# Kernel optimization log

Measured on AMD Instinct MI355X. Metric: run time of the kernel, lower is better.

The kernel has to match this reference:

```python
import jax, jax.numpy as jnp
import numpy as np

D = 512      # d_model
H = 8        # n_head
NL = 3       # encoder layers
FF = 2048    # torch TransformerEncoderLayer default dim_feedforward
HID = 256    # hidden_size
ACT = 12     # action_size
NOBJ = 89    # num_objects
BAND = 17    # tril(diagonal=-17) -> keys older than 16 steps banned


def setup_inputs() -> dict:
    key = jax.random.key(0)
    ks = iter(jax.random.split(key, 48))
    rn = lambda shape, s=0.02: jax.random.normal(next(ks), shape, jnp.float32) * s
    b, seq = 16, 512
    inp = {
        'state_input': jax.random.normal(next(ks), (b, seq, 3, 16, 16), jnp.float32),
        'goal_input': jax.random.normal(next(ks), (b, seq, 300), jnp.float32),
        # encoders (stand-ins for obs_enc / lang_enc)
        'W_obs': rn((256, 3 * 16 * 16)), 'b_obs': rn((256,)),
        'W_lang': rn((256, 300)), 'b_lang': rn((256,)),
        # input projection 512 -> 512
        'W_in': rn((D, 512)), 'b_in': rn((D,)),
        # per-layer transformer params, stacked on layer dim
        'Wqkv': rn((NL, 3 * D, D)), 'bqkv': rn((NL, 3 * D)),
        'Wo': rn((NL, D, D)), 'bo': rn((NL, D)),
        'W1': rn((NL, FF, D)), 'b1': rn((NL, FF)),
        'W2': rn((NL, D, FF)), 'b2': rn((NL, D)),
        'g1': jnp.ones((NL, D)), 'bt1': jnp.zeros((NL, D)),
        'g2': jnp.ones((NL, D)), 'bt2': jnp.zeros((NL, D)),
        # output heads
        'W_outp': rn((HID, D)), 'b_outp': rn((HID,)),
        'W_a1': rn((ACT, HID)), 'b_a1': rn((ACT,)),
        'W_a2': rn((NOBJ, HID)), 'b_a2': rn((NOBJ,)),
    }
    return inp


def _ln(y, g, bt):
    m = y.mean(-1, keepdims=True)
    v = y.var(-1, keepdims=True)
    return (y - m) / jnp.sqrt(v + 1e-5) * g + bt


def _encoder(x, mask_add, Wqkv, bqkv, Wo, bo, W1, b1, W2, b2, g1, bt1, g2, bt2):
    b, n, _ = x.shape
    dh = D // H
    scale = 1.0 / np.sqrt(dh)
    for l in range(NL):
        qkv = x @ Wqkv[l].T + bqkv[l]
        q, k, v = jnp.split(qkv, 3, axis=-1)
        hd = lambda t: t.reshape(b, n, H, dh).transpose(0, 2, 1, 3)  # [b,h,n,dh]
        q, k, v = hd(q), hd(k), hd(v)
        sc = jnp.einsum('bhqd,bhkd->bhqk', q, k) * scale + mask_add
        a = jax.nn.softmax(sc, axis=-1)
        o = jnp.einsum('bhqk,bhkd->bhqd', a, v).transpose(0, 2, 1, 3).reshape(b, n, D)
        o = o @ Wo[l].T + bo[l]
        x = _ln(x + o, g1[l], bt1[l])             # post-LN (torch default)
        f = jax.nn.relu(x @ W1[l].T + b1[l]) @ W2[l].T + b2[l]
        x = _ln(x + f, g2[l], bt2[l])
    return x


def reference(state_input, goal_input, W_obs, b_obs, W_lang, b_lang, W_in, b_in,
              Wqkv, bqkv, Wo, bo, W1, b1, W2, b2, g1, bt1, g2, bt2,
              W_outp, b_outp, W_a1, b_a1, W_a2, b_a2):
    b, s = state_input.shape[:2]
    st = state_input.reshape(b, s, -1) @ W_obs.T + b_obs          # obs_enc
    lg = goal_input @ W_lang.T + b_lang                            # lang_enc
    x = jnp.concatenate([st, lg], axis=-1) @ W_in.T + b_in        # [b,s,D]
    # key padding mask; sentinel token appended (causal_mask=False branch)
    pad = ~jnp.any(goal_input != -1, axis=-1)                      # [b,s]
    pad = jnp.concatenate([pad, jnp.zeros((b, 1), bool)], axis=1)
    x = jnp.concatenate([x, jnp.zeros((b, 1, D), x.dtype)], axis=1)
    n = s + 1
    i = jnp.arange(n)
    # banned: tril(-17) | triu(1)  -> attend only to keys in [i-16, i]
    mask2 = ((i[:, None] - i[None, :]) >= BAND) | (i[None, :] > i[:, None])
    banned = mask2[None, None, :, :] | pad[:, None, None, :]
    mask_add = jnp.where(banned, jnp.float32(-1e9), jnp.float32(0.0))
    x = _encoder(x, mask_add, Wqkv, bqkv, Wo, bo, W1, b1, W2, b2, g1, bt1, g2, bt2)
    out = x[:, :-1, :]                                             # drop sentinel
    h = out @ W_outp.T + b_outp
    l1 = h @ W_a1.T + b_a1
    l2 = h @ W_a2.T + b_a2
    return jnp.concatenate([l1, l2], axis=-1)                      # [b,s,101]
```

## Files before the change

kernel.cpp:

```cpp
#include <hip/hip_runtime.h>

#define D 512
#define H 8
#define NL 3
#define FFD 2048
#define HID 256
#define BAND 17
#define BATCH 16
#define SEQ 512
#define MTOK (BATCH * SEQ)
#define NOUT 101
#define NOUTP 128

typedef unsigned short u16;
typedef __attribute__((ext_vector_type(8))) short short8;
typedef __attribute__((ext_vector_type(4))) float f32x4;
typedef __attribute__((ext_vector_type(8))) unsigned short u16x8;

__device__ inline float bf2f(u16 u) {
    union { unsigned int i; float f; } x; x.i = ((unsigned int)u) << 16; return x.f;
}
__device__ inline u16 f2bf(float f) {
    union { float f; unsigned int i; } x; x.f = f;
    unsigned int r = x.i + 0x7fffu + ((x.i >> 16) & 1u);
    return (u16)(r >> 16);
}

__device__ __forceinline__ void gload_lds16(const u16* g, u16* l) {
    __builtin_amdgcn_global_load_lds(
        (const __attribute__((address_space(1))) unsigned int*)(g),
        (__attribute__((address_space(3))) unsigned int*)(l),
        16, 0, 0);
}

#define BM 128
#define BN 128
#define BK 32

__global__ __launch_bounds__(512) void gemm_kernel(
    const u16* __restrict__ A, int lda,
    const u16* __restrict__ B, int ldb,
    const float* __restrict__ bias,
    float* __restrict__ Cf0, float* __restrict__ Cf1, int ldcf,
    u16* __restrict__ Cb, int ldcb,
    int M, int N, int K, int relu)
{
    __shared__ u16 As[3][BM * BK];
    __shared__ u16 Bs[3][BN * BK];
    const int tid  = threadIdx.x;
    const int lane = tid & 63;
    const int wv   = tid >> 6;
    const int wr = wv >> 2, wc = wv & 3;

    const int nb  = gridDim.x * gridDim.y;
    const int bid = blockIdx.y * gridDim.x + blockIdx.x;
    const int tile = (bid & 7) * (nb >> 3) + (bid >> 3);
    const int m0 = (tile / gridDim.x) * BM;
    const int n0 = (tile % gridDim.x) * BN;
    const int kz = blockIdx.z * K;

    f32x4 acc[4][2] = {};

    const int srow = lane >> 2;
    const int schunk = (lane & 3) ^ (srow & 3);
    const size_t aoff = (size_t)(m0 + wv * 16 + srow) * lda + kz + schunk * 8;
    const size_t boff = (size_t)(n0 + wv * 16 + srow) * ldb + kz + schunk * 8;

    const int frow = lane & 15;
    const int q    = lane >> 4;
    const int rcol = ((q ^ (frow & 3)) << 3);

    #define STAGE(buf, k0)                                             \
        do {                                                           \
            gload_lds16(A + aoff + (k0), &As[buf][wv * 16 * BK]);      \
            gload_lds16(B + boff + (k0), &Bs[buf][wv * 16 * BK]);      \
        } while (0)

    #define COMPUTE(buf)                                                            \
        do {                                                                        \
            short8 af[4], bf[2];                                                    \
            _Pragma("unroll")                                                       \
            for (int i = 0; i < 4; ++i)                                             \
                af[i] = *(const short8*)&As[buf][(wr * 64 + i * 16 + frow) * BK + rcol]; \
            _Pragma("unroll")                                                       \
            for (int j = 0; j < 2; ++j)                                             \
                bf[j] = *(const short8*)&Bs[buf][(wc * 32 + j * 16 + frow) * BK + rcol]; \
            _Pragma("unroll")                                                       \
            for (int i = 0; i < 4; ++i)                                             \
                _Pragma("unroll")                                                   \
                for (int j = 0; j < 2; ++j)                                         \
                    acc[i][j] = __builtin_amdgcn_mfma_f32_16x16x32_bf16(            \
                        af[i], bf[j], acc[i][j], 0, 0, 0);                          \
        } while (0)

    const int nt = K >> 5;
    STAGE(0, 0);
    STAGE(1, 32);
    int cur = 0;
    for (int t = 0; t < nt - 2; ++t) {
        int s = cur + 2; if (s >= 3) s -= 3;
        STAGE(s, (t + 2) << 5);
        asm volatile("s_waitcnt vmcnt(4)" ::: "memory");
        __builtin_amdgcn_s_barrier();
        __builtin_amdgcn_sched_barrier(0);
        COMPUTE(cur);
        __builtin_amdgcn_s_barrier();
        ++cur; if (cur >= 3) cur = 0;
    }
    asm volatile("s_waitcnt vmcnt(2)" ::: "memory");
    __builtin_amdgcn_s_barrier();
    __builtin_amdgcn_sched_barrier(0);
    COMPUTE(cur);
    __builtin_amdgcn_s_barrier();
    ++cur; if (cur >= 3) cur = 0;
    asm volatile("s_waitcnt vmcnt(0)" ::: "memory");
    __builtin_amdgcn_s_barrier();
    __builtin_amdgcn_sched_barrier(0);
    COMPUTE(cur);

    #undef STAGE
    #undef COMPUTE

    float* Cf = blockIdx.z ? Cf1 : Cf0;
    const bool addb = (bias != nullptr) && (blockIdx.z == 0);

    const int crow0 = (lane >> 4) * 4;
    const int ccol  = lane & 15;
    #pragma unroll
    for (int j = 0; j < 2; ++j) {
        int gcol = n0 + wc * 32 + j * 16 + ccol;
        if (gcol >= N) continue;
        float bv = addb ? bias[gcol] : 0.f;
        #pragma unroll
        for (int i = 0; i < 4; ++i) {
            #pragma unroll
            for (int r = 0; r < 4; ++r) {
                int grow = m0 + wr * 64 + i * 16 + crow0 + r;
                float v = acc[i][j][r] + bv;
                if (relu) v = fmaxf(v, 0.f);
                if (Cf) Cf[(size_t)grow * ldcf + gcol] = v;
                if (Cb) Cb[(size_t)grow * ldcb + gcol] = f2bf(v);
            }
        }
    }
}

#define CHUNK 128
#define KSLOT 144
#define VT_LD 152

__global__ __launch_bounds__(512) void attn_kernel(
    const u16* __restrict__ qkv, const unsigned char* __restrict__ pad,
    u16* __restrict__ o)
{
    __shared__ u16 Vt[64 * VT_LD];
    __shared__ u16 Pl[8 * 16 * 40];
    __shared__ unsigned char padl[KSLOT];

    const int tid = threadIdx.x, lane = tid & 63, wv = tid >> 6;
    const int b = blockIdx.z, h = blockIdx.y, c0 = blockIdx.x * CHUNK;
    const u16* base = qkv + (size_t)b * SEQ * (3 * D);

    for (int s = tid; s < KSLOT * 4; s += 512) {
        int t = s >> 2, dq = (s & 3) * 16;
        int j = c0 - 16 + t; if (j < 0) j = 0;
        const u16* vrow = base + (size_t)j * (3 * D) + 2 * D + h * 64 + dq;
        u16 tmp[16];
        *(u16x8*)&tmp[0] = *(const u16x8*)&vrow[0];
        *(u16x8*)&tmp[8] = *(const u16x8*)&vrow[8];
        #pragma unroll
        for (int d = 0; d < 16; ++d)
            Vt[(dq + d) * VT_LD + t] = tmp[d];
    }
    if (tid < KSLOT) {
        int j = c0 - 16 + tid;
        padl[tid] = (j >= 0) ? pad[b * SEQ + j] : (unsigned char)1;
    }
    __syncthreads();

    const int qi0 = wv * 16;
    const int i0  = c0 + qi0;
    const int frow = lane & 15;
    const int g    = lane >> 4;
    const int kg8  = g * 8;
    const int g4   = g * 4;

    short8 qf[2];
    #pragma unroll
    for (int kk = 0; kk < 2; ++kk)
        qf[kk] = *(const short8*)&base[(size_t)(i0 + frow) * (3 * D) + h * 64 + kk * 32 + kg8];

    f32x4 sacc[2] = {};
    #pragma unroll
    for (int jb = 0; jb < 2; ++jb) {
        int jrow = i0 - 16 + jb * 16 + frow; if (jrow < 0) jrow = 0;
        const u16* kbase = base + (size_t)jrow * (3 * D) + D + h * 64;
        #pragma unroll
        for (int kk = 0; kk < 2; ++kk) {
            short8 kf = *(const short8*)&kbase[kk * 32 + kg8];
            sacc[jb] = __builtin_amdgcn_mfma_f32_16x16x32_bf16(qf[kk], kf, sacc[jb], 0, 0, 0);
        }
    }

    float sv[2][4];
    #pragma unroll
    for (int jb = 0; jb < 2; ++jb) {
        int s = jb * 16 + frow;
        int jg = i0 - 16 + s;
        bool padk = (jg < 0) || padl[qi0 + s];
        #pragma unroll
        for (int r = 0; r < 4; ++r) {
            int qq = g4 + r;
            bool banned = (s < qq) || (s > qq + 16) || padk;
            sv[jb][r] = sacc[jb][r] * 0.125f + (banned ? -1e9f : 0.f);
        }
    }

    float ex[2][4], rdn[4];
    #pragma unroll
    for (int r = 0; r < 4; ++r) {
        float m = fmaxf(sv[0][r], sv[1][r]);
        #pragma unroll
        for (int off = 1; off < 16; off <<= 1) m = fmaxf(m, __shfl_xor(m, off));
        float e0 = __expf(sv[0][r] - m);
        float e1 = __expf(sv[1][r] - m);
        float dsum = e0 + e1;
        #pragma unroll
        for (int off = 1; off < 16; off <<= 1) dsum += __shfl_xor(dsum, off);
        ex[0][r] = e0; ex[1][r] = e1;
        rdn[r] = 1.f / dsum;
    }

    u16* Pw = &Pl[wv * 640];
    #pragma unroll
    for (int jb = 0; jb < 2; ++jb)
        #pragma unroll
        for (int r = 0; r < 4; ++r)
            Pw[(g4 + r) * 40 + jb * 16 + frow] = f2bf(ex[jb][r]);
    short8 pa = *(const short8*)&Pw[frow * 40 + kg8];

    f32x4 oacc[4] = {};
    #pragma unroll
    for (int nb = 0; nb < 4; ++nb) {
        short8 vf = *(const short8*)&Vt[(nb * 16 + frow) * VT_LD + qi0 + kg8];
        oacc[nb] = __builtin_amdgcn_mfma_f32_16x16x32_bf16(pa, vf, oacc[nb], 0, 0, 0);
    }

    #pragma unroll
    for (int r = 0; r < 4; ++r) {
        size_t row = (size_t)(b * SEQ + i0 + g4 + r);
        #pragma unroll
        for (int nb = 0; nb < 4; ++nb)
            o[row * D + h * 64 + nb * 16 + frow] = f2bf(oacc[nb][r] * rdn[r]);
    }
}

__global__ __launch_bounds__(256) void resln_kernel(
    const u16* __restrict__ xin,
    const float* __restrict__ d0, const float* __restrict__ d1,
    const float* __restrict__ g, const float* __restrict__ bt,
    u16* __restrict__ xb)
{
    int row  = blockIdx.x * 4 + (threadIdx.x >> 6);
    int lane = threadIdx.x & 63;
    const f32x4* r0 = (const f32x4*)(d0 + (size_t)row * D);
    const f32x4* r1 = (const f32x4*)(d1 + (size_t)row * D);
    u16x8 xv = *(const u16x8*)(xin + (size_t)row * D + lane * 8);

    f32x4 y0 = r0[lane * 2]     + r1[lane * 2];
    f32x4 y1 = r0[lane * 2 + 1] + r1[lane * 2 + 1];
    #pragma unroll
    for (int c = 0; c < 4; ++c) { y0[c] += bf2f(xv[c]); y1[c] += bf2f(xv[c + 4]); }

    float s = 0.f, s2 = 0.f;
    #pragma unroll
    for (int c = 0; c < 4; ++c) {
        s  += y0[c] + y1[c];
        s2 += y0[c] * y0[c] + y1[c] * y1[c];
    }
    #pragma unroll
    for (int off = 32; off > 0; off >>= 1) {
        s  += __shfl_xor(s, off);
        s2 += __shfl_xor(s2, off);
    }
    float mean = s * (1.f / D);
    float var  = s2 * (1.f / D) - mean * mean;
    float inv  = rsqrtf(fmaxf(var, 0.f) + 1e-5f);

    f32x4 gv0 = ((const f32x4*)g)[lane * 2],  gv1 = ((const f32x4*)g)[lane * 2 + 1];
    f32x4 bv0 = ((const f32x4*)bt)[lane * 2], bv1 = ((const f32x4*)bt)[lane * 2 + 1];
    u16x8 ob;
    #pragma unroll
    for (int c = 0; c < 4; ++c) {
        ob[c]     = f2bf((y0[c] - mean) * inv * gv0[c] + bv0[c]);
        ob[c + 4] = f2bf((y1[c] - mean) * inv * gv1[c] + bv1[c]);
    }
    *(u16x8*)(xb + (size_t)row * D + lane * 8) = ob;
}

__global__ __launch_bounds__(256) void pad_kernel(
    const float* __restrict__ goal, unsigned char* __restrict__ pad)
{
    int row  = blockIdx.x * 4 + (threadIdx.x >> 6);
    int lane = threadIdx.x & 63;
    const f32x4* gr = (const f32x4*)(goal + (size_t)row * 300);
    bool any = false;
    for (int c4 = lane; c4 < 75; c4 += 64) {
        f32x4 v = gr[c4];
        any |= (v[0] != -1.f) | (v[1] != -1.f) | (v[2] != -1.f) | (v[3] != -1.f);
    }
    unsigned long long b = __ballot(any);
    if (lane == 0) pad[row] = (b == 0ull) ? 1 : 0;
}

struct CvtJob { const float* src; u16* dstb; float* dstf; int n; int mode; };
struct CvtArgs { CvtJob j[15]; int blk0[16]; };

__global__ __launch_bounds__(256) void cvt_kernel(CvtArgs a) {
    const int bx = blockIdx.x;
    int jid = 0;
    #pragma unroll 1
    while (jid < 14 && bx >= a.blk0[jid + 1]) ++jid;
    const CvtJob jb = a.j[jid];
    const int i0 = (bx - a.blk0[jid]) * 2048 + threadIdx.x * 8;
    if (i0 >= jb.n) return;

    if (jb.mode == 0) {
        if (i0 + 8 <= jb.n) {
            f32x4 v0 = *(const f32x4*)(jb.src + i0);
            f32x4 v1 = *(const f32x4*)(jb.src + i0 + 4);
            u16x8 o;
            #pragma unroll
            for (int c = 0; c < 4; ++c) { o[c] = f2bf(v0[c]); o[c + 4] = f2bf(v1[c]); }
            *(u16x8*)(jb.dstb + i0) = o;
        } else {
            for (int e = 0; e < 8 && i0 + e < jb.n; ++e) jb.dstb[i0 + e] = f2bf(jb.src[i0 + e]);
        }
    } else if (jb.mode == 2) {
        int r = (int)((unsigned)i0 / 320u);
        int c = i0 - r * 320;
        const float* s = jb.src + (size_t)r * 300 + c;
        u16x8 o;
        if (c + 8 <= 300) {
            f32x4 v0 = *(const f32x4*)s;
            f32x4 v1 = *(const f32x4*)(s + 4);
            #pragma unroll
            for (int cc = 0; cc < 4; ++cc) { o[cc] = f2bf(v0[cc]); o[cc + 4] = f2bf(v1[cc]); }
        } else {
            #pragma unroll
            for (int e = 0; e < 8; ++e) o[e] = (c + e < 300) ? f2bf(s[e]) : (u16)0;
        }
        *(u16x8*)(jb.dstb + i0) = o;
    } else if (jb.mode == 1) {
        for (int e = 0; e < 8 && i0 + e < jb.n; ++e) jb.dstf[i0 + e] = jb.src[i0 + e];
    } else {
        u16x8 z = {0, 0, 0, 0, 0, 0, 0, 0};
        *(u16x8*)(jb.dstb + i0) = z;
    }
}


extern "C" void kernel_launch(void* const* d_in, const int* in_sizes, int n_in,
                              void* d_out, int out_size, void* d_ws, size_t ws_size,
                              hipStream_t stream)
{
    const float* state  = (const float*)d_in[0];
    const float* goal   = (const float*)d_in[1];
    const float* W_obs  = (const float*)d_in[2];
    const float* b_obs  = (const float*)d_in[3];
    const float* W_lang = (const float*)d_in[4];
    const float* b_lang = (const float*)d_in[5];
    const float* W_in   = (const float*)d_in[6];
    const float* b_in   = (const float*)d_in[7];
    const float* Wqkv   = (const float*)d_in[8];
    const float* bqkv   = (const float*)d_in[9];
    const float* Wo     = (const float*)d_in[10];
    const float* bo     = (const float*)d_in[11];
    const float* W1     = (const float*)d_in[12];
    const float* b1     = (const float*)d_in[13];
    const float* W2     = (const float*)d_in[14];
    const float* b2     = (const float*)d_in[15];
    const float* g1     = (const float*)d_in[16];
    const float* bt1    = (const float*)d_in[17];
    const float* g2     = (const float*)d_in[18];
    const float* bt2    = (const float*)d_in[19];
    const float* W_outp = (const float*)d_in[20];
    const float* b_outp = (const float*)d_in[21];
    const float* W_a1   = (const float*)d_in[22];
    const float* b_a1   = (const float*)d_in[23];
    const float* W_a2   = (const float*)d_in[24];
    const float* b_a2   = (const float*)d_in[25];

    char* ws = (char*)d_ws;
    size_t off = 0;
    auto alloc = [&](size_t bytes) -> void* {
        void* p = ws + off;
        off = (off + bytes + 255) & ~(size_t)255;
        return p;
    };

    u16* wqkv_b  = (u16*)alloc((size_t)NL * 1536 * D * 2);
    u16* wo_b    = (u16*)alloc((size_t)NL * D * D * 2);
    u16* w1_b    = (u16*)alloc((size_t)NL * FFD * D * 2);
    u16* w2_b    = (u16*)alloc((size_t)NL * D * FFD * 2);
    u16* wobs_b  = (u16*)alloc((size_t)256 * 768 * 2);
    u16* wlang_b = (u16*)alloc((size_t)256 * 320 * 2);
    u16* win_b   = (u16*)alloc((size_t)D * D * 2);
    u16* woutp_b = (u16*)alloc((size_t)HID * D * 2);
    u16* wa_b    = (u16*)alloc((size_t)NOUTP * HID * 2);
    float* ba_f  = (float*)alloc((size_t)NOUT * 4);
    u16* state_b = (u16*)alloc((size_t)MTOK * 768 * 2);
    u16* goal_b  = (u16*)alloc((size_t)MTOK * 320 * 2);
    u16* feat_b  = (u16*)alloc((size_t)MTOK * D * 2);
    u16* x_b     = (u16*)alloc((size_t)MTOK * D * 2);
    u16* qkv_b   = (u16*)alloc((size_t)MTOK * 3 * D * 2);
    u16* o_b     = (u16*)alloc((size_t)MTOK * D * 2);
    float* delta_f = (float*)alloc((size_t)MTOK * D * 4);
    u16* h1_b    = (u16*)alloc((size_t)MTOK * FFD * 2);
    u16* hout_b  = (u16*)alloc((size_t)MTOK * HID * 2);
    unsigned char* pad_u8 = (unsigned char*)alloc(MTOK);
    float* delta2_f = (float*)state_b;
    (void)ws_size; (void)in_sizes; (void)n_in; (void)out_size;

    CvtArgs ca;
    int nj = 0, blks = 0;
    auto addj = [&](const float* s, u16* db, float* df, int n, int mode) {
        ca.j[nj].src = s; ca.j[nj].dstb = db; ca.j[nj].dstf = df;
        ca.j[nj].n = n; ca.j[nj].mode = mode;
        ca.blk0[nj] = blks;
        blks += (n + 2047) / 2048;
        ++nj;
    };
    addj(state,  state_b, nullptr, MTOK * 768, 0);
    addj(goal,   goal_b,  nullptr, MTOK * 320, 2);
    addj(Wqkv,   wqkv_b,  nullptr, NL * 1536 * D, 0);
    addj(Wo,     wo_b,    nullptr, NL * D * D, 0);
    addj(W1,     w1_b,    nullptr, NL * FFD * D, 0);
    addj(W2,     w2_b,    nullptr, NL * D * FFD, 0);
    addj(W_obs,  wobs_b,  nullptr, 256 * 768, 0);
    addj(W_lang, wlang_b, nullptr, 256 * 320, 2);
    addj(W_in,   win_b,   nullptr, D * D, 0);
    addj(W_outp, woutp_b, nullptr, HID * D, 0);
    addj(W_a1,   wa_b,            nullptr, 12 * HID, 0);
    addj(W_a2,   wa_b + 12 * HID, nullptr, 89 * HID, 0);
    addj(nullptr, wa_b + NOUT * HID, nullptr, (NOUTP - NOUT) * HID, 3);
    addj(b_a1,   nullptr, ba_f,      12, 1);
    addj(b_a2,   nullptr, ba_f + 12, 89, 1);
    ca.blk0[nj] = blks;
    cvt_kernel<<<blks, 256, 0, stream>>>(ca);

    pad_kernel<<<MTOK / 4, 256, 0, stream>>>(goal, pad_u8);

    auto gemm = [&](const u16* A, int lda, const u16* B, int ldb, const float* bias,
                    float* Cf0, float* Cf1, int ldcf, u16* Cb, int ldcb,
                    int N, int K, int relu, int ksplit) {
        dim3 grid((N + BN - 1) / BN, MTOK / BM, ksplit);
        gemm_kernel<<<grid, 512, 0, stream>>>(A, lda, B, ldb, bias, Cf0, Cf1, ldcf,
                                              Cb, ldcb, MTOK, N, K / ksplit, relu);
    };

    gemm(state_b, 768, wobs_b, 768, b_obs, nullptr, nullptr, 0, feat_b, D, 256, 768, 0, 1);
    gemm(goal_b, 320, wlang_b, 320, b_lang, nullptr, nullptr, 0, feat_b + 256, D, 256, 320, 0, 1);
    gemm(feat_b, D, win_b, D, b_in, nullptr, nullptr, 0, x_b, D, D, D, 0, 1);

    for (int l = 0; l < NL; ++l) {
        gemm(x_b, D, wqkv_b + (size_t)l * 1536 * D, D, bqkv + l * 1536,
             nullptr, nullptr, 0, qkv_b, 3 * D, 3 * D, D, 0, 1);
        {
            dim3 grid(SEQ / CHUNK, H, BATCH);
            attn_kernel<<<grid, 512, 0, stream>>>(qkv_b, pad_u8, o_b);
        }
        gemm(o_b, D, wo_b + (size_t)l * D * D, D, bo + l * D,
             delta_f, delta2_f, D, nullptr, 0, D, D, 0, 2);
        resln_kernel<<<MTOK / 4, 256, 0, stream>>>(x_b, delta_f, delta2_f,
                                                   g1 + l * D, bt1 + l * D, x_b);
        gemm(x_b, D, w1_b + (size_t)l * FFD * D, D, b1 + l * FFD,
             nullptr, nullptr, 0, h1_b, FFD, FFD, D, 1, 1);
        gemm(h1_b, FFD, w2_b + (size_t)l * D * FFD, FFD, b2 + l * D,
             delta_f, delta2_f, D, nullptr, 0, D, FFD, 0, 2);
        resln_kernel<<<MTOK / 4, 256, 0, stream>>>(x_b, delta_f, delta2_f,
                                                   g2 + l * D, bt2 + l * D, x_b);
    }

    gemm(x_b, D, woutp_b, D, b_outp, nullptr, nullptr, 0, hout_b, HID, HID, D, 0, 1);
    gemm(hout_b, HID, wa_b, HID, ba_f, (float*)d_out, nullptr, NOUT, nullptr, 0, NOUT, HID, 0, 1);
}
```

Measured before the change: 433.4 us.

## Use 4-wave GEMM blocks with 64x64 warp tiles and bf16 split-K partials

The GEMM moves from 8 waves to 4 waves per 128x128 block. Each wave now covers a 64x64 sub-tile and issues twice as many global-to-LDS loads, which raises MFMA reuse per LDS fragment load. The split-K partial outputs of the Wo and W2 GEMMs are now stored as bf16 instead of fp32, and the residual+LayerNorm kernel reads them as bf16, halving that traffic. In exchange, accumulator register pressure rises and the partial sums lose precision.

```diff
diff --git a/kernel.cpp b/kernel.cpp
--- a/kernel.cpp
+++ b/kernel.cpp
@@ -37,12 +37,12 @@
 #define BN 128
 #define BK 32
 
-__global__ __launch_bounds__(512) void gemm_kernel(
+__global__ __launch_bounds__(256) void gemm_kernel(
     const u16* __restrict__ A, int lda,
     const u16* __restrict__ B, int ldb,
     const float* __restrict__ bias,
-    float* __restrict__ Cf0, float* __restrict__ Cf1, int ldcf,
-    u16* __restrict__ Cb, int ldcb,
+    float* __restrict__ Cf, int ldcf,
+    u16* __restrict__ Cb0, u16* __restrict__ Cb1, int ldcb,
     int M, int N, int K, int relu)
 {
     __shared__ u16 As[3][BM * BK];
@@ -50,7 +50,7 @@
     const int tid  = threadIdx.x;
     const int lane = tid & 63;
     const int wv   = tid >> 6;
-    const int wr = wv >> 2, wc = wv & 3;
+    const int wr = wv >> 1, wc = wv & 1;
 
     const int nb  = gridDim.x * gridDim.y;
     const int bid = blockIdx.y * gridDim.x + blockIdx.x;
@@ -59,36 +59,40 @@
     const int n0 = (tile % gridDim.x) * BN;
     const int kz = blockIdx.z * K;
 
-    f32x4 acc[4][2] = {};
+    f32x4 acc[4][4] = {};
 
     const int srow = lane >> 2;
     const int schunk = (lane & 3) ^ (srow & 3);
-    const size_t aoff = (size_t)(m0 + wv * 16 + srow) * lda + kz + schunk * 8;
-    const size_t boff = (size_t)(n0 + wv * 16 + srow) * ldb + kz + schunk * 8;
+    const size_t aoff0 = (size_t)(m0 + (wv * 2 + 0) * 16 + srow) * lda + kz + schunk * 8;
+    const size_t aoff1 = (size_t)(m0 + (wv * 2 + 1) * 16 + srow) * lda + kz + schunk * 8;
+    const size_t boff0 = (size_t)(n0 + (wv * 2 + 0) * 16 + srow) * ldb + kz + schunk * 8;
+    const size_t boff1 = (size_t)(n0 + (wv * 2 + 1) * 16 + srow) * ldb + kz + schunk * 8;
 
     const int frow = lane & 15;
     const int q    = lane >> 4;
     const int rcol = ((q ^ (frow & 3)) << 3);
 
-    #define STAGE(buf, k0)                                             \
-        do {                                                           \
-            gload_lds16(A + aoff + (k0), &As[buf][wv * 16 * BK]);      \
-            gload_lds16(B + boff + (k0), &Bs[buf][wv * 16 * BK]);      \
+    #define STAGE(buf, k0)                                                  \
+        do {                                                                \
+            gload_lds16(A + aoff0 + (k0), &As[buf][(wv * 2 + 0) * 512]);    \
+            gload_lds16(A + aoff1 + (k0), &As[buf][(wv * 2 + 1) * 512]);    \
+            gload_lds16(B + boff0 + (k0), &Bs[buf][(wv * 2 + 0) * 512]);    \
+            gload_lds16(B + boff1 + (k0), &Bs[buf][(wv * 2 + 1) * 512]);    \
         } while (0)
 
     #define COMPUTE(buf)                                                            \
         do {                                                                        \
-            short8 af[4], bf[2];                                                    \
+            short8 af[4], bf[4];                                                    \
             _Pragma("unroll")                                                       \
             for (int i = 0; i < 4; ++i)                                             \
                 af[i] = *(const short8*)&As[buf][(wr * 64 + i * 16 + frow) * BK + rcol]; \
             _Pragma("unroll")                                                       \
-            for (int j = 0; j < 2; ++j)                                             \
-                bf[j] = *(const short8*)&Bs[buf][(wc * 32 + j * 16 + frow) * BK + rcol]; \
+            for (int j = 0; j < 4; ++j)                                             \
+                bf[j] = *(const short8*)&Bs[buf][(wc * 64 + j * 16 + frow) * BK + rcol]; \
             _Pragma("unroll")                                                       \
             for (int i = 0; i < 4; ++i)                                             \
                 _Pragma("unroll")                                                   \
-                for (int j = 0; j < 2; ++j)                                         \
+                for (int j = 0; j < 4; ++j)                                         \
                     acc[i][j] = __builtin_amdgcn_mfma_f32_16x16x32_bf16(            \
                         af[i], bf[j], acc[i][j], 0, 0, 0);                          \
         } while (0)
@@ -100,14 +104,14 @@
     for (int t = 0; t < nt - 2; ++t) {
         int s = cur + 2; if (s >= 3) s -= 3;
         STAGE(s, (t + 2) << 5);
-        asm volatile("s_waitcnt vmcnt(4)" ::: "memory");
+        asm volatile("s_waitcnt vmcnt(8)" ::: "memory");
         __builtin_amdgcn_s_barrier();
         __builtin_amdgcn_sched_barrier(0);
         COMPUTE(cur);
         __builtin_amdgcn_s_barrier();
         ++cur; if (cur >= 3) cur = 0;
     }
-    asm volatile("s_waitcnt vmcnt(2)" ::: "memory");
+    asm volatile("s_waitcnt vmcnt(4)" ::: "memory");
     __builtin_amdgcn_s_barrier();
     __builtin_amdgcn_sched_barrier(0);
     COMPUTE(cur);
@@ -121,14 +125,14 @@
     #undef STAGE
     #undef COMPUTE
 
-    float* Cf = blockIdx.z ? Cf1 : Cf0;
+    u16* Cb = blockIdx.z ? Cb1 : Cb0;
     const bool addb = (bias != nullptr) && (blockIdx.z == 0);
 
     const int crow0 = (lane >> 4) * 4;
     const int ccol  = lane & 15;
     #pragma unroll
-    for (int j = 0; j < 2; ++j) {
-        int gcol = n0 + wc * 32 + j * 16 + ccol;
+    for (int j = 0; j < 4; ++j) {
+        int gcol = n0 + wc * 64 + j * 16 + ccol;
         if (gcol >= N) continue;
         float bv = addb ? bias[gcol] : 0.f;
         #pragma unroll
@@ -257,26 +261,22 @@
 
 __global__ __launch_bounds__(256) void resln_kernel(
     const u16* __restrict__ xin,
-    const float* __restrict__ d0, const float* __restrict__ d1,
+    const u16* __restrict__ d0, const u16* __restrict__ d1,
     const float* __restrict__ g, const float* __restrict__ bt,
     u16* __restrict__ xb)
 {
     int row  = blockIdx.x * 4 + (threadIdx.x >> 6);
     int lane = threadIdx.x & 63;
-    const f32x4* r0 = (const f32x4*)(d0 + (size_t)row * D);
-    const f32x4* r1 = (const f32x4*)(d1 + (size_t)row * D);
     u16x8 xv = *(const u16x8*)(xin + (size_t)row * D + lane * 8);
-
-    f32x4 y0 = r0[lane * 2]     + r1[lane * 2];
-    f32x4 y1 = r0[lane * 2 + 1] + r1[lane * 2 + 1];
-    #pragma unroll
-    for (int c = 0; c < 4; ++c) { y0[c] += bf2f(xv[c]); y1[c] += bf2f(xv[c + 4]); }
-
+    u16x8 dv0 = *(const u16x8*)(d0 + (size_t)row * D + lane * 8);
+    u16x8 dv1 = *(const u16x8*)(d1 + (size_t)row * D + lane * 8);
+
+    float y[8];
     float s = 0.f, s2 = 0.f;
     #pragma unroll
-    for (int c = 0; c < 4; ++c) {
-        s  += y0[c] + y1[c];
-        s2 += y0[c] * y0[c] + y1[c] * y1[c];
+    for (int c = 0; c < 8; ++c) {
+        y[c] = bf2f(xv[c]) + bf2f(dv0[c]) + bf2f(dv1[c]);
+        s += y[c]; s2 += y[c] * y[c];
     }
     #pragma unroll
     for (int off = 32; off > 0; off >>= 1) {
@@ -292,8 +292,8 @@
     u16x8 ob;
     #pragma unroll
     for (int c = 0; c < 4; ++c) {
-        ob[c]     = f2bf((y0[c] - mean) * inv * gv0[c] + bv0[c]);
-        ob[c + 4] = f2bf((y1[c] - mean) * inv * gv1[c] + bv1[c]);
+        ob[c]     = f2bf((y[c] - mean) * inv * gv0[c] + bv0[c]);
+        ob[c + 4] = f2bf((y[c + 4] - mean) * inv * gv1[c] + bv1[c]);
     }
     *(u16x8*)(xb + (size_t)row * D + lane * 8) = ob;
 }
@@ -415,11 +415,11 @@
     u16* x_b     = (u16*)alloc((size_t)MTOK * D * 2);
     u16* qkv_b   = (u16*)alloc((size_t)MTOK * 3 * D * 2);
     u16* o_b     = (u16*)alloc((size_t)MTOK * D * 2);
-    float* delta_f = (float*)alloc((size_t)MTOK * D * 4);
+    u16* delta_b = (u16*)alloc((size_t)MTOK * D * 2);
     u16* h1_b    = (u16*)alloc((size_t)MTOK * FFD * 2);
     u16* hout_b  = (u16*)alloc((size_t)MTOK * HID * 2);
     unsigned char* pad_u8 = (unsigned char*)alloc(MTOK);
-    float* delta2_f = (float*)state_b;
+    u16* delta2_b = state_b;
     (void)ws_size; (void)in_sizes; (void)n_in; (void)out_size;
 
     CvtArgs ca;
@@ -452,36 +452,36 @@
     pad_kernel<<<MTOK / 4, 256, 0, stream>>>(goal, pad_u8);
 
     auto gemm = [&](const u16* A, int lda, const u16* B, int ldb, const float* bias,
-                    float* Cf0, float* Cf1, int ldcf, u16* Cb, int ldcb,
+                    float* Cf, int ldcf, u16* Cb0, u16* Cb1, int ldcb,
                     int N, int K, int relu, int ksplit) {
         dim3 grid((N + BN - 1) / BN, MTOK / BM, ksplit);
-        gemm_kernel<<<grid, 512, 0, stream>>>(A, lda, B, ldb, bias, Cf0, Cf1, ldcf,
-                                              Cb, ldcb, MTOK, N, K / ksplit, relu);
+        gemm_kernel<<<grid, 256, 0, stream>>>(A, lda, B, ldb, bias, Cf, ldcf,
+                                              Cb0, Cb1, ldcb, MTOK, N, K / ksplit, relu);
     };
 
-    gemm(state_b, 768, wobs_b, 768, b_obs, nullptr, nullptr, 0, feat_b, D, 256, 768, 0, 1);
-    gemm(goal_b, 320, wlang_b, 320, b_lang, nullptr, nullptr, 0, feat_b + 256, D, 256, 320, 0, 1);
-    gemm(feat_b, D, win_b, D, b_in, nullptr, nullptr, 0, x_b, D, D, D, 0, 1);
+    gemm(state_b, 768, wobs_b, 768, b_obs, nullptr, 0, feat_b, nullptr, D, 256, 768, 0, 1);
+    gemm(goal_b, 320, wlang_b, 320, b_lang, nullptr, 0, feat_b + 256, nullptr, D, 256, 320, 0, 1);
+    gemm(feat_b, D, win_b, D, b_in, nullptr, 0, x_b, nullptr, D, D, D, 0, 1);
 
     for (int l = 0; l < NL; ++l) {
         gemm(x_b, D, wqkv_b + (size_t)l * 1536 * D, D, bqkv + l * 1536,
-             nullptr, nullptr, 0, qkv_b, 3 * D, 3 * D, D, 0, 1);
+             nullptr, 0, qkv_b, nullptr, 3 * D, 3 * D, D, 0, 1);
         {
             dim3 grid(SEQ / CHUNK, H, BATCH);
             attn_kernel<<<grid, 512, 0, stream>>>(qkv_b, pad_u8, o_b);
         }
         gemm(o_b, D, wo_b + (size_t)l * D * D, D, bo + l * D,
-             delta_f, delta2_f, D, nullptr, 0, D, D, 0, 2);
-        resln_kernel<<<MTOK / 4, 256, 0, stream>>>(x_b, delta_f, delta2_f,
+             nullptr, 0, delta_b, delta2_b, D, D, D, 0, 2);
+        resln_kernel<<<MTOK / 4, 256, 0, stream>>>(x_b, delta_b, delta2_b,
                                                    g1 + l * D, bt1 + l * D, x_b);
         gemm(x_b, D, w1_b + (size_t)l * FFD * D, D, b1 + l * FFD,
-             nullptr, nullptr, 0, h1_b, FFD, FFD, D, 1, 1);
+             nullptr, 0, h1_b, nullptr, FFD, FFD, D, 1, 1);
         gemm(h1_b, FFD, w2_b + (size_t)l * D * FFD, FFD, b2 + l * D,
-             delta_f, delta2_f, D, nullptr, 0, D, FFD, 0, 2);
-        resln_kernel<<<MTOK / 4, 256, 0, stream>>>(x_b, delta_f, delta2_f,
+             nullptr, 0, delta_b, delta2_b, D, D, FFD, 0, 2);
+        resln_kernel<<<MTOK / 4, 256, 0, stream>>>(x_b, delta_b, delta2_b,
                                                    g2 + l * D, bt2 + l * D, x_b);
     }
 
-    gemm(x_b, D, woutp_b, D, b_outp, nullptr, nullptr, 0, hout_b, HID, HID, D, 0, 1);
-    gemm(hout_b, HID, wa_b, HID, ba_f, (float*)d_out, nullptr, NOUT, nullptr, 0, NOUT, HID, 0, 1);
-}
+    gemm(x_b, D, woutp_b, D, b_outp, nullptr, 0, hout_b, nullptr, HID, HID, D, 0, 1);
+    gemm(hout_b, HID, wa_b, HID, ba_f, (float*)d_out, NOUT, nullptr, nullptr, 0, NOUT, HID, 0, 1);
+}
```

Measured after the change: 458.7 us. +5.8%, slower.
